# Optimization experiments

Measured on AMD Instinct MI355X. Metric: run time of the kernel, lower is better.

## Reference

```python
import jax, jax.numpy as jnp
import numpy as np

EPS = 1.1920929e-07  # torch nn.RMSNorm default eps = finfo(float32).eps
COS_EPS = 1e-8       # torch F.cosine_similarity denominator clamp

def rms_norm(x):
    # nn.RMSNorm(head_dim, elementwise_affine=False)
    return x / jnp.sqrt(jnp.mean(x * x, axis=-1, keepdims=True) + EPS)

def slerp(low, high, val):
    # spherical interpolation per last dim
    cos = jnp.sum(low * high, -1) / jnp.maximum(
        jnp.linalg.norm(low, axis=-1) * jnp.linalg.norm(high, axis=-1), COS_EPS)
    omega = jnp.arccos(jnp.clip(cos, -1.0 + 1e-7, 1.0 - 1e-7))[..., None]
    so = jnp.sin(omega)
    return (low * jnp.sin((1.0 - val) * omega) + high * jnp.sin(val * omega)) / so

def setup_inputs() -> dict:
    key = jax.random.key(0)
    k1, k2 = jax.random.split(key)
    z = jax.random.normal(k1, (8, 512, 2048), jnp.float32)          # [B, D, L]
    codebooks = rms_norm(jax.random.normal(k2, (8, 1024, 64), jnp.float32))  # [H, M, d]
    return {"z": z, "codebooks": codebooks}

def reference(z, codebooks, commitment_cost=0.25, decay=0.99):
    B, D, L = z.shape
    H, M, d = codebooks.shape
    # rearrange 'b (h d) l -> h (b l) d'
    z_split = z.reshape(B, H, d, L).transpose(1, 0, 3, 2).reshape(H, B * L, d)  # [H, N, d]

    sim = jnp.einsum('hnd,hmd->hnm', z_split, codebooks)          # [H, N, M]
    indices = jnp.argmax(sim, axis=-1)                            # [H, N]
    z_split_q = jnp.take_along_axis(codebooks, indices[:, :, None], axis=1)  # [H, N, d]

    commitment_loss = jnp.mean((jax.lax.stop_gradient(z_split) - z_split_q) ** 2)
    codebook_loss = jnp.mean((z_split - jax.lax.stop_gradient(z_split_q)) ** 2)
    vq_loss = codebook_loss + commitment_cost * commitment_loss

    # EMA slerp codebook update (training path, no_grad) -- vectorized over unique-code loop
    zs = jax.lax.stop_gradient(z_split)
    sums = jax.vmap(lambda zh, ih: jax.ops.segment_sum(zh, ih, num_segments=M))(zs, indices)  # [H, M, d]
    counts = jax.vmap(lambda ih: jax.ops.segment_sum(jnp.ones(ih.shape, zs.dtype), ih, num_segments=M))(indices)  # [H, M]
    means = sums / jnp.maximum(counts, 1.0)[..., None]
    updated = rms_norm(slerp(means, codebooks, decay))
    new_codebooks = jnp.where(counts[..., None] > 0, updated, codebooks)

    # rearrange back 'h (b l) d -> b (h d) l' and 'h (b l) -> b h l'
    z_q = z_split_q.reshape(H, B, L, d).transpose(1, 0, 3, 2).reshape(B, D, L)
    indices_out = indices.reshape(H, B, L).transpose(1, 0, 2)
    z_q = z + jax.lax.stop_gradient(z_q - z)  # straight-through
    return z_q, vq_loss, indices_out, new_codebooks
```

## Files before the change

### kernel.cpp

```cpp
#include <hip/hip_runtime.h>
#include <hip/hip_bf16.h>
#include <math.h>

#define BZ   8
#define DD   512
#define LL   2048
#define HH   8
#define MM   1024
#define DH   64
#define NN   (BZ * LL)
#define TOTAL_ELEMS (HH * NN * DH)

#define OFF_ZQ   0
#define OFF_LOSS 8388608
#define OFF_IDX  8388609
#define OFF_CB   8519681

#define CAP  128

#define WSB_SSE    0
#define WSB_CNT    64
#define WSB_LST    (64 + HH * MM * 4)
#define WSB_CBHI   (WSB_LST + HH * MM * CAP * 2)
#define WSB_CBLO   (WSB_CBHI + HH * MM * DH * 2)
#define WSB_ZS     (WSB_CBLO + HH * MM * DH * 2)
#define WS_NEED_BUCKET ((size_t)WSB_ZS + (size_t)HH * NN * DH * 4)

#define WS_PLANES_BYTE 64
#define WS_ZSPLIT_BYTE (64 + 2u * HH * MM * DH * 2)
#define WS_NEED_FAT    (WS_ZSPLIT_BYTE + (size_t)HH * NN * DH * 4)

typedef __attribute__((ext_vector_type(8))) short short8;
typedef __attribute__((ext_vector_type(4))) float float4v;

__device__ __forceinline__ unsigned short f2bf(float f) {
    unsigned int u = __builtin_bit_cast(unsigned int, f);
    u += 0x7FFFu + ((u >> 16) & 1u);
    return (unsigned short)(u >> 16);
}
__device__ __forceinline__ float bf2f(unsigned short s) {
    unsigned int u = ((unsigned int)s) << 16;
    return __builtin_bit_cast(float, u);
}

__device__ __forceinline__ void gload16(const short* g, short* l) {
    __builtin_amdgcn_global_load_lds(
        (const __attribute__((address_space(1))) unsigned int*)g,
        (__attribute__((address_space(3))) unsigned int*)l, 16, 0, 0);
}

__global__ __launch_bounds__(256) void cvt_cb_kernel(
    const float* __restrict__ cb, short* __restrict__ hip_, short* __restrict__ lop_)
{
    const int tid = blockIdx.x * 256 + threadIdx.x;
    const int c   = tid & 7;
    const int row = tid >> 3;
    const float* __restrict__ src = cb + (size_t)row * DH + c * 8;
    short hs[8], ls[8];
#pragma unroll
    for (int j = 0; j < 8; ++j) {
        const float f = src[j];
        const unsigned short hv = f2bf(f);
        hs[j] = (short)hv;
        ls[j] = (short)f2bf(f - bf2f(hv));
    }
    const int dst = row * DH + ((c ^ (row & 7)) * 8);
    *(short8*)&hip_[dst] = *(short8*)hs;
    *(short8*)&lop_[dst] = *(short8*)ls;
}

__global__ __launch_bounds__(512) void vq_assign_kernel(
    const float* __restrict__ z,
    const float* __restrict__ cb,
    const short* __restrict__ cb_hi,
    const short* __restrict__ cb_lo,
    float* __restrict__ zq_out,
    float* __restrict__ idx_out,
    float* __restrict__ sse,
    float* __restrict__ zs,
    int*   __restrict__ cnts,
    unsigned short* __restrict__ lists)
{
    __shared__ __align__(16) short hi_lds[2][64 * DH];
    __shared__ __align__(16) short lo_lds[2][64 * DH];
    __shared__ float blk_err[8];

    const int t    = threadIdx.x;
    const int h    = blockIdx.y;
    const int lane = t & 63;
    const int g    = lane >> 4;
    const int nloc = lane & 15;
    const int w    = t >> 6;

    const int r = blockIdx.x * 128 + w * 16 + nloc;
    const int b = r >> 11;
    const int l = r & (LL - 1);
    const float* __restrict__ zbase = z + ((size_t)(b * DD + h * DH) * LL + l);

    float zv[16] __attribute__((aligned(16)));
#pragma unroll
    for (int j = 0; j < 8; ++j) zv[j]     = zbase[(size_t)(g * 8 + j) * LL];
#pragma unroll
    for (int j = 0; j < 8; ++j) zv[8 + j] = zbase[(size_t)(32 + g * 8 + j) * LL];

    if (zs) {
        float* __restrict__ zr_ = zs + ((size_t)h * NN + r) * DH;
        *(float4*)&zr_[g * 8]          = *(const float4*)&zv[0];
        *(float4*)&zr_[g * 8 + 4]      = *(const float4*)&zv[4];
        *(float4*)&zr_[32 + g * 8]     = *(const float4*)&zv[8];
        *(float4*)&zr_[32 + g * 8 + 4] = *(const float4*)&zv[12];
    }

    short bh[16], bl[16];
#pragma unroll
    for (int j = 0; j < 16; ++j) {
        const unsigned short hv = f2bf(zv[j]);
        bh[j] = (short)hv;
        bl[j] = (short)f2bf(zv[j] - bf2f(hv));
    }
    const short8 Bh0 = *(short8*)&bh[0], Bh1 = *(short8*)&bh[8];
    const short8 Bl0 = *(short8*)&bl[0], Bl1 = *(short8*)&bl[8];

    const short* __restrict__ gh = cb_hi + (size_t)h * MM * DH;
    const short* __restrict__ gl = cb_lo + (size_t)h * MM * DH;

    auto stage = [&](int mt, int buf) {
        const short* sh = gh + (size_t)mt * 64 * DH;
        const short* sl = gl + (size_t)mt * 64 * DH;
        gload16(sh + t * 8, &hi_lds[buf][t * 8]);
        gload16(sl + t * 8, &lo_lds[buf][t * 8]);
    };

    stage(0, 0);

    float b1c[4], b2c[4];
    int   i1c[4], i2c[4];
#pragma unroll
    for (int s = 0; s < 4; ++s) { b1c[s] = -1e30f; b2c[s] = -1e30f; i1c[s] = 0; i2c[s] = 0; }

    const int sw8 = nloc & 7;

    for (int mt = 0; mt < MM / 64; ++mt) {
        __syncthreads();
        if (mt + 1 < MM / 64) stage(mt + 1, (mt + 1) & 1);
        const int buf = mt & 1;

#pragma unroll
        for (int s = 0; s < 4; ++s) {
            const short* hrow = &hi_lds[buf][(s * 16 + nloc) * DH];
            const short* lrow = &lo_lds[buf][(s * 16 + nloc) * DH];
            const short8 Ah0 = *(const short8*)&hrow[((g)     ^ sw8) * 8];
            const short8 Ah1 = *(const short8*)&hrow[((g + 4) ^ sw8) * 8];
            const short8 Al0 = *(const short8*)&lrow[((g)     ^ sw8) * 8];
            const short8 Al1 = *(const short8*)&lrow[((g + 4) ^ sw8) * 8];

            float4v acc = {0.f, 0.f, 0.f, 0.f};
            acc = __builtin_amdgcn_mfma_f32_16x16x32_bf16(Ah0, Bh0, acc, 0, 0, 0);
            acc = __builtin_amdgcn_mfma_f32_16x16x32_bf16(Ah1, Bh1, acc, 0, 0, 0);
            acc = __builtin_amdgcn_mfma_f32_16x16x32_bf16(Ah0, Bl0, acc, 0, 0, 0);
            acc = __builtin_amdgcn_mfma_f32_16x16x32_bf16(Ah1, Bl1, acc, 0, 0, 0);
            acc = __builtin_amdgcn_mfma_f32_16x16x32_bf16(Al0, Bh0, acc, 0, 0, 0);
            acc = __builtin_amdgcn_mfma_f32_16x16x32_bf16(Al1, Bh1, acc, 0, 0, 0);

            const int mbase = mt * 64 + s * 16 + g * 4;
#pragma unroll
            for (int reg = 0; reg < 4; ++reg) {
                const float v = acc[reg];
                const int   m = mbase + reg;
                const bool gt1 = v > b1c[s];
                const bool gt2 = v > b2c[s];
                b2c[s] = __builtin_amdgcn_fmed3f(v, b1c[s], b2c[s]);
                i2c[s] = gt1 ? i1c[s] : (gt2 ? m : i2c[s]);
                b1c[s] = fmaxf(v, b1c[s]);
                i1c[s] = gt1 ? m : i1c[s];
            }
        }
    }

    float b1 = b1c[0], b2 = b2c[0];
    int   i1 = i1c[0], i2 = i2c[0];
#pragma unroll
    for (int s = 1; s < 4; ++s) {
        const float ob1 = b1c[s], ob2 = b2c[s];
        const int   oi1 = i1c[s], oi2 = i2c[s];
        const bool agt = (b1 > ob1) || (b1 == ob1 && i1 < oi1);
        const float w1 = agt ? b1 : ob1;  const int wi1 = agt ? i1 : oi1;
        const float l1 = agt ? ob1 : b1;  const int li1 = agt ? oi1 : i1;
        const float w2 = agt ? b2 : ob2;  const int wi2 = agt ? i2 : oi2;
        const bool sgt = (l1 > w2) || (l1 == w2 && li1 < wi2);
        b1 = w1;  i1 = wi1;
        b2 = sgt ? l1 : w2;  i2 = sgt ? li1 : wi2;
    }

#pragma unroll
    for (int off = 16; off <= 32; off <<= 1) {
        float ob1 = __shfl_xor(b1, off, 64);
        int   oi1 = __shfl_xor(i1, off, 64);
        float ob2 = __shfl_xor(b2, off, 64);
        int   oi2 = __shfl_xor(i2, off, 64);
        const bool agt = (b1 > ob1) || (b1 == ob1 && i1 < oi1);
        const float w1  = agt ? b1 : ob1;  const int wi1 = agt ? i1 : oi1;
        const float l1  = agt ? ob1 : b1;  const int li1 = agt ? oi1 : i1;
        const float w2  = agt ? b2 : ob2;  const int wi2 = agt ? i2 : oi2;
        const bool sgt = (l1 > w2) || (l1 == w2 && li1 < wi2);
        b1 = w1;  i1 = wi1;
        b2 = sgt ? l1 : w2;  i2 = sgt ? li1 : wi2;
    }

    const float* __restrict__ cbh = cb + (size_t)h * MM * DH;
    const float* __restrict__ c1  = cbh + (size_t)i1 * DH;
    const float* __restrict__ c2  = cbh + (size_t)i2 * DH;
    double d1 = 0.0, d2 = 0.0;
#pragma unroll
    for (int j = 0; j < 8; ++j) {
        const int k0 = g * 8 + j, k1 = 32 + g * 8 + j;
        d1 = fma((double)zv[j],     (double)c1[k0], d1);
        d1 = fma((double)zv[8 + j], (double)c1[k1], d1);
        d2 = fma((double)zv[j],     (double)c2[k0], d2);
        d2 = fma((double)zv[8 + j], (double)c2[k1], d2);
    }
    d1 += __shfl_xor(d1, 16, 64);  d1 += __shfl_xor(d1, 32, 64);
    d2 += __shfl_xor(d2, 16, 64);  d2 += __shfl_xor(d2, 32, 64);
    const int best = (d2 > d1 || (d2 == d1 && i2 < i1)) ? i2 : i1;

    const float* __restrict__ cq  = cbh + (size_t)best * DH;
    float* __restrict__ zqp  = zq_out + ((size_t)(b * DD + h * DH) * LL + l);
    float err = 0.f;
#pragma unroll
    for (int j = 0; j < 8; ++j) {
        const int k0 = g * 8 + j, k1 = 32 + g * 8 + j;
        const float q0 = cq[k0], q1 = cq[k1];
        zqp[(size_t)k0 * LL] = q0;
        zqp[(size_t)k1 * LL] = q1;
        const float e0 = zv[j] - q0, e1 = zv[8 + j] - q1;
        err = fmaf(e0, e0, err);
        err = fmaf(e1, e1, err);
    }
    if (g == 0) {
        idx_out[((size_t)b * HH + h) * LL + l] = (float)best;
        if (cnts) {
            const int code = h * MM + best;
            const int slot = atomicAdd(&cnts[code], 1);
            if (slot < CAP) lists[(size_t)code * CAP + slot] = (unsigned short)r;
        }
    }
#pragma unroll
    for (int off = 32; off; off >>= 1) err += __shfl_xor(err, off, 64);
    if (lane == 0) blk_err[w] = err;
    __syncthreads();
    if (t == 0) {
        float s = 0.f;
#pragma unroll
        for (int i = 0; i < 8; ++i) s += blk_err[i];
        atomicAdd(sse, s);
    }
}

__global__ __launch_bounds__(256) void vq_update_kernel(
    const float* __restrict__ z,
    const float* __restrict__ zs,
    const float* __restrict__ cb,
    const float* __restrict__ idx,
    const float* __restrict__ sse,
    float* __restrict__ cb_out,
    float* __restrict__ loss_out,
    const int* __restrict__ cnts,
    const unsigned short* __restrict__ lists)
{
    if (blockIdx.x == 0 && threadIdx.x == 0) {
        loss_out[0] = 1.25f * sse[0] / (float)TOTAL_ELEMS;
    }
    const int row  = blockIdx.x * 4 + (threadIdx.x >> 6);
    const int lane = threadIdx.x & 63;
    const int h    = row >> 10;
    const int m    = row & (MM - 1);
    const float fm = (float)m;

    float acc = 0.f;
    int   cnt = 0;
    bool  fast = false;
    if (cnts) { cnt = cnts[row]; fast = (cnt <= CAP); }

    if (fast) {
        const unsigned short* __restrict__ lst = lists + (size_t)row * CAP;
        const float* __restrict__ zsh = zs + ((size_t)h * NN) * DH + lane;
        float a0 = 0.f, a1 = 0.f, a2 = 0.f, a3 = 0.f;
        int i = 0;
        for (; i + 4 <= cnt; i += 4) {
            const int n0 = lst[i], n1 = lst[i + 1], n2 = lst[i + 2], n3 = lst[i + 3];
            a0 += zsh[(size_t)n0 * DH];
            a1 += zsh[(size_t)n1 * DH];
            a2 += zsh[(size_t)n2 * DH];
            a3 += zsh[(size_t)n3 * DH];
        }
        for (; i < cnt; ++i) acc += zsh[(size_t)lst[i] * DH];
        acc += (a0 + a1) + (a2 + a3);
    } else {
        cnt = 0;
#pragma unroll 1
        for (int b = 0; b < BZ; ++b) {
            const float* __restrict__ ip  = idx + ((size_t)(b * HH + h)) * LL;
            const float* __restrict__ zb  = z + ((size_t)(b * DD + h * DH + lane)) * LL;
            const float* __restrict__ zsb = zs ? (zs + ((size_t)h * NN + (size_t)b * LL) * DH + lane)
                                              : (const float*)0;
            float4 cur = *(const float4*)(ip + lane * 4);
#pragma unroll 1
            for (int it = 0; it < LL / 256; ++it) {
                float4 nxt = cur;
                if (it + 1 < LL / 256)
                    nxt = *(const float4*)(ip + (it + 1) * 256 + lane * 4);
#pragma unroll
                for (int j = 0; j < 4; ++j) {
                    const float ivj = (&cur.x)[j];
                    unsigned long long mask = __ballot(ivj == fm);
                    cnt += (int)__popcll(mask);
                    while (mask) {
                        const int src = (int)__ffsll((long long)mask) - 1;
                        mask &= mask - 1;
                        const int l = it * 256 + src * 4 + j;
                        acc += zsb ? zsb[(size_t)l * DH]
                                   : zb[l];
                    }
                }
                cur = nxt;
            }
        }
    }

    const float cf   = (float)cnt;
    const float c    = cb[(size_t)row * DH + lane];
    const float mean = acc / fmaxf(cf, 1.0f);

    float dot = mean * c;
    float nl  = mean * mean;
    float nh  = c * c;
#pragma unroll
    for (int off = 32; off; off >>= 1) {
        dot += __shfl_xor(dot, off, 64);
        nl  += __shfl_xor(nl,  off, 64);
        nh  += __shfl_xor(nh,  off, 64);
    }

    float cosv = dot / fmaxf(sqrtf(nl) * sqrtf(nh), 1e-8f);
    cosv = fminf(fmaxf(cosv, -0.9999999f), 0.9999999f);
    const float omega = acosf(cosv);
    const float so    = sinf(omega);
    float outv = (mean * sinf(0.01f * omega) + c * sinf(0.99f * omega)) / so;

    float ms = outv * outv;
#pragma unroll
    for (int off = 32; off; off >>= 1) ms += __shfl_xor(ms, off, 64);
    ms = ms * (1.0f / (float)DH) + 1.1920929e-07f;
    const float normed = outv / sqrtf(ms);

    cb_out[(size_t)row * DH + lane] = (cnt > 0) ? normed : c;
}

extern "C" void kernel_launch(void* const* d_in, const int* in_sizes, int n_in,
                              void* d_out, int out_size, void* d_ws, size_t ws_size,
                              hipStream_t stream) {
    const float* z  = (const float*)d_in[0];
    const float* cb = (const float*)d_in[1];
    float* out = (float*)d_out;

    const bool bucket = ws_size >= WS_NEED_BUCKET;
    const bool fat    = ws_size >= WS_NEED_FAT;

    short *cb_hi, *cb_lo;
    float *zs = 0;
    int   *cnts = 0;
    unsigned short *lists = 0;

    if (bucket) {
        cnts  = (int*)((char*)d_ws + WSB_CNT);
        lists = (unsigned short*)((char*)d_ws + WSB_LST);
        cb_hi = (short*)((char*)d_ws + WSB_CBHI);
        cb_lo = (short*)((char*)d_ws + WSB_CBLO);
        zs    = (float*)((char*)d_ws + WSB_ZS);
        hipMemsetAsync(d_ws, 0, WSB_LST, stream);
    } else {
        cb_hi = (short*)((char*)d_ws + WS_PLANES_BYTE);
        cb_lo = cb_hi + (size_t)HH * MM * DH;
        zs    = fat ? (float*)((char*)d_ws + WS_ZSPLIT_BYTE) : (float*)0;
        hipMemsetAsync(d_ws, 0, 64, stream);
    }

    cvt_cb_kernel<<<(HH * MM * DH / 8) / 256, 256, 0, stream>>>(cb, cb_hi, cb_lo);

    dim3 gridA(NN / 128, HH);
    vq_assign_kernel<<<gridA, 512, 0, stream>>>(
        z, cb, cb_hi, cb_lo,
        out + OFF_ZQ, out + OFF_IDX, (float*)d_ws, zs, cnts, lists);

    dim3 gridB((HH * MM) / 4);
    vq_update_kernel<<<gridB, 256, 0, stream>>>(
        z, zs, cb, out + OFF_IDX, (float*)d_ws,
        out + OFF_CB, out + OFF_LOSS, cnts, lists);
}
```

Baseline: 190.5 us.

## Process two row tiles per wave to reuse staged codebook fragments

```diff
diff --git a/kernel.cpp b/kernel.cpp
--- a/kernel.cpp
+++ b/kernel.cpp
@@ -69,7 +69,7 @@
     *(short8*)&lop_[dst] = *(short8*)ls;
 }
 
-__global__ __launch_bounds__(512) void vq_assign_kernel(
+__global__ __launch_bounds__(512, 4) void vq_assign_kernel(
     const float* __restrict__ z,
     const float* __restrict__ cb,
     const short* __restrict__ cb_hi,
@@ -92,34 +92,39 @@
     const int nloc = lane & 15;
     const int w    = t >> 6;
 
-    const int r = blockIdx.x * 128 + w * 16 + nloc;
-    const int b = r >> 11;
-    const int l = r & (LL - 1);
-    const float* __restrict__ zbase = z + ((size_t)(b * DD + h * DH) * LL + l);
-
-    float zv[16] __attribute__((aligned(16)));
-#pragma unroll
-    for (int j = 0; j < 8; ++j) zv[j]     = zbase[(size_t)(g * 8 + j) * LL];
-#pragma unroll
-    for (int j = 0; j < 8; ++j) zv[8 + j] = zbase[(size_t)(32 + g * 8 + j) * LL];
-
-    if (zs) {
-        float* __restrict__ zr_ = zs + ((size_t)h * NN + r) * DH;
-        *(float4*)&zr_[g * 8]          = *(const float4*)&zv[0];
-        *(float4*)&zr_[g * 8 + 4]      = *(const float4*)&zv[4];
-        *(float4*)&zr_[32 + g * 8]     = *(const float4*)&zv[8];
-        *(float4*)&zr_[32 + g * 8 + 4] = *(const float4*)&zv[12];
-    }
-
-    short bh[16], bl[16];
-#pragma unroll
-    for (int j = 0; j < 16; ++j) {
-        const unsigned short hv = f2bf(zv[j]);
-        bh[j] = (short)hv;
-        bl[j] = (short)f2bf(zv[j] - bf2f(hv));
-    }
-    const short8 Bh0 = *(short8*)&bh[0], Bh1 = *(short8*)&bh[8];
-    const short8 Bl0 = *(short8*)&bl[0], Bl1 = *(short8*)&bl[8];
+    const int rbase = blockIdx.x * 256 + w * 32;
+
+    short8 Bh0[2], Bh1[2], Bl0[2], Bl1[2];
+#pragma unroll
+    for (int u = 0; u < 2; ++u) {
+        const int r = rbase + u * 16 + nloc;
+        const int b = r >> 11;
+        const int l = r & (LL - 1);
+        const float* __restrict__ zbase = z + ((size_t)(b * DD + h * DH) * LL + l);
+        float zv[16] __attribute__((aligned(16)));
+#pragma unroll
+        for (int j = 0; j < 8; ++j) zv[j]     = zbase[(size_t)(g * 8 + j) * LL];
+#pragma unroll
+        for (int j = 0; j < 8; ++j) zv[8 + j] = zbase[(size_t)(32 + g * 8 + j) * LL];
+
+        if (zs) {
+            float* __restrict__ zr_ = zs + ((size_t)h * NN + r) * DH;
+            *(float4*)&zr_[g * 8]          = *(const float4*)&zv[0];
+            *(float4*)&zr_[g * 8 + 4]      = *(const float4*)&zv[4];
+            *(float4*)&zr_[32 + g * 8]     = *(const float4*)&zv[8];
+            *(float4*)&zr_[32 + g * 8 + 4] = *(const float4*)&zv[12];
+        }
+
+        short bh[16], bl[16];
+#pragma unroll
+        for (int j = 0; j < 16; ++j) {
+            const unsigned short hv = f2bf(zv[j]);
+            bh[j] = (short)hv;
+            bl[j] = (short)f2bf(zv[j] - bf2f(hv));
+        }
+        Bh0[u] = *(short8*)&bh[0];  Bh1[u] = *(short8*)&bh[8];
+        Bl0[u] = *(short8*)&bl[0];  Bl1[u] = *(short8*)&bl[8];
+    }
 
     const short* __restrict__ gh = cb_hi + (size_t)h * MM * DH;
     const short* __restrict__ gl = cb_lo + (size_t)h * MM * DH;
@@ -136,7 +141,7 @@
     float b1c[4], b2c[4];
     int   i1c[4], i2c[4];
 #pragma unroll
-    for (int s = 0; s < 4; ++s) { b1c[s] = -1e30f; b2c[s] = -1e30f; i1c[s] = 0; i2c[s] = 0; }
+    for (int c = 0; c < 4; ++c) { b1c[c] = -1e30f; b2c[c] = -1e30f; i1c[c] = 0; i2c[c] = 0; }
 
     const int sw8 = nloc & 7;
 
@@ -154,99 +159,128 @@
             const short8 Al0 = *(const short8*)&lrow[((g)     ^ sw8) * 8];
             const short8 Al1 = *(const short8*)&lrow[((g + 4) ^ sw8) * 8];
 
-            float4v acc = {0.f, 0.f, 0.f, 0.f};
-            acc = __builtin_amdgcn_mfma_f32_16x16x32_bf16(Ah0, Bh0, acc, 0, 0, 0);
-            acc = __builtin_amdgcn_mfma_f32_16x16x32_bf16(Ah1, Bh1, acc, 0, 0, 0);
-            acc = __builtin_amdgcn_mfma_f32_16x16x32_bf16(Ah0, Bl0, acc, 0, 0, 0);
-            acc = __builtin_amdgcn_mfma_f32_16x16x32_bf16(Ah1, Bl1, acc, 0, 0, 0);
-            acc = __builtin_amdgcn_mfma_f32_16x16x32_bf16(Al0, Bh0, acc, 0, 0, 0);
-            acc = __builtin_amdgcn_mfma_f32_16x16x32_bf16(Al1, Bh1, acc, 0, 0, 0);
-
             const int mbase = mt * 64 + s * 16 + g * 4;
 #pragma unroll
-            for (int reg = 0; reg < 4; ++reg) {
-                const float v = acc[reg];
-                const int   m = mbase + reg;
-                const bool gt1 = v > b1c[s];
-                const bool gt2 = v > b2c[s];
-                b2c[s] = __builtin_amdgcn_fmed3f(v, b1c[s], b2c[s]);
-                i2c[s] = gt1 ? i1c[s] : (gt2 ? m : i2c[s]);
-                b1c[s] = fmaxf(v, b1c[s]);
-                i1c[s] = gt1 ? m : i1c[s];
+            for (int u = 0; u < 2; ++u) {
+                float4v acc = {0.f, 0.f, 0.f, 0.f};
+                acc = __builtin_amdgcn_mfma_f32_16x16x32_bf16(Ah0, Bh0[u], acc, 0, 0, 0);
+                acc = __builtin_amdgcn_mfma_f32_16x16x32_bf16(Ah1, Bh1[u], acc, 0, 0, 0);
+                acc = __builtin_amdgcn_mfma_f32_16x16x32_bf16(Ah0, Bl0[u], acc, 0, 0, 0);
+                acc = __builtin_amdgcn_mfma_f32_16x16x32_bf16(Ah1, Bl1[u], acc, 0, 0, 0);
+                acc = __builtin_amdgcn_mfma_f32_16x16x32_bf16(Al0, Bh0[u], acc, 0, 0, 0);
+                acc = __builtin_amdgcn_mfma_f32_16x16x32_bf16(Al1, Bh1[u], acc, 0, 0, 0);
+
+#pragma unroll
+                for (int reg = 0; reg < 4; ++reg) {
+                    const int   c = u * 2 + (reg & 1);
+                    const float v = acc[reg];
+                    const int   m = mbase + reg;
+                    const bool gt1 = v > b1c[c];
+                    const bool gt2 = v > b2c[c];
+                    b2c[c] = __builtin_amdgcn_fmed3f(v, b1c[c], b2c[c]);
+                    i2c[c] = gt1 ? i1c[c] : (gt2 ? m : i2c[c]);
+                    b1c[c] = fmaxf(v, b1c[c]);
+                    i1c[c] = gt1 ? m : i1c[c];
+                }
             }
         }
     }
 
-    float b1 = b1c[0], b2 = b2c[0];
-    int   i1 = i1c[0], i2 = i2c[0];
-#pragma unroll
-    for (int s = 1; s < 4; ++s) {
-        const float ob1 = b1c[s], ob2 = b2c[s];
-        const int   oi1 = i1c[s], oi2 = i2c[s];
-        const bool agt = (b1 > ob1) || (b1 == ob1 && i1 < oi1);
-        const float w1 = agt ? b1 : ob1;  const int wi1 = agt ? i1 : oi1;
-        const float l1 = agt ? ob1 : b1;  const int li1 = agt ? oi1 : i1;
-        const float w2 = agt ? b2 : ob2;  const int wi2 = agt ? i2 : oi2;
-        const bool sgt = (l1 > w2) || (l1 == w2 && li1 < wi2);
-        b1 = w1;  i1 = wi1;
-        b2 = sgt ? l1 : w2;  i2 = sgt ? li1 : wi2;
-    }
-
-#pragma unroll
-    for (int off = 16; off <= 32; off <<= 1) {
-        float ob1 = __shfl_xor(b1, off, 64);
-        int   oi1 = __shfl_xor(i1, off, 64);
-        float ob2 = __shfl_xor(b2, off, 64);
-        int   oi2 = __shfl_xor(i2, off, 64);
-        const bool agt = (b1 > ob1) || (b1 == ob1 && i1 < oi1);
-        const float w1  = agt ? b1 : ob1;  const int wi1 = agt ? i1 : oi1;
-        const float l1  = agt ? ob1 : b1;  const int li1 = agt ? oi1 : i1;
-        const float w2  = agt ? b2 : ob2;  const int wi2 = agt ? i2 : oi2;
-        const bool sgt = (l1 > w2) || (l1 == w2 && li1 < wi2);
-        b1 = w1;  i1 = wi1;
-        b2 = sgt ? l1 : w2;  i2 = sgt ? li1 : wi2;
-    }
-
     const float* __restrict__ cbh = cb + (size_t)h * MM * DH;
-    const float* __restrict__ c1  = cbh + (size_t)i1 * DH;
-    const float* __restrict__ c2  = cbh + (size_t)i2 * DH;
-    double d1 = 0.0, d2 = 0.0;
-#pragma unroll
-    for (int j = 0; j < 8; ++j) {
-        const int k0 = g * 8 + j, k1 = 32 + g * 8 + j;
-        d1 = fma((double)zv[j],     (double)c1[k0], d1);
-        d1 = fma((double)zv[8 + j], (double)c1[k1], d1);
-        d2 = fma((double)zv[j],     (double)c2[k0], d2);
-        d2 = fma((double)zv[8 + j], (double)c2[k1], d2);
-    }
-    d1 += __shfl_xor(d1, 16, 64);  d1 += __shfl_xor(d1, 32, 64);
-    d2 += __shfl_xor(d2, 16, 64);  d2 += __shfl_xor(d2, 32, 64);
-    const int best = (d2 > d1 || (d2 == d1 && i2 < i1)) ? i2 : i1;
-
-    const float* __restrict__ cq  = cbh + (size_t)best * DH;
-    float* __restrict__ zqp  = zq_out + ((size_t)(b * DD + h * DH) * LL + l);
-    float err = 0.f;
-#pragma unroll
-    for (int j = 0; j < 8; ++j) {
-        const int k0 = g * 8 + j, k1 = 32 + g * 8 + j;
-        const float q0 = cq[k0], q1 = cq[k1];
-        zqp[(size_t)k0 * LL] = q0;
-        zqp[(size_t)k1 * LL] = q1;
-        const float e0 = zv[j] - q0, e1 = zv[8 + j] - q1;
-        err = fmaf(e0, e0, err);
-        err = fmaf(e1, e1, err);
-    }
-    if (g == 0) {
-        idx_out[((size_t)b * HH + h) * LL + l] = (float)best;
-        if (cnts) {
-            const int code = h * MM + best;
-            const int slot = atomicAdd(&cnts[code], 1);
-            if (slot < CAP) lists[(size_t)code * CAP + slot] = (unsigned short)r;
-        }
-    }
-#pragma unroll
-    for (int off = 32; off; off >>= 1) err += __shfl_xor(err, off, 64);
-    if (lane == 0) blk_err[w] = err;
+    float err_total = 0.f;
+
+#pragma unroll
+    for (int u = 0; u < 2; ++u) {
+        float b1 = b1c[u * 2], b2 = b2c[u * 2];
+        int   i1 = i1c[u * 2], i2 = i2c[u * 2];
+        {
+            const float ob1 = b1c[u * 2 + 1], ob2 = b2c[u * 2 + 1];
+            const int   oi1 = i1c[u * 2 + 1], oi2 = i2c[u * 2 + 1];
+            const bool agt = (b1 > ob1) || (b1 == ob1 && i1 < oi1);
+            const float w1 = agt ? b1 : ob1;  const int wi1 = agt ? i1 : oi1;
+            const float l1 = agt ? ob1 : b1;  const int li1 = agt ? oi1 : i1;
+            const float w2 = agt ? b2 : ob2;  const int wi2 = agt ? i2 : oi2;
+            const bool sgt = (l1 > w2) || (l1 == w2 && li1 < wi2);
+            b1 = w1;  i1 = wi1;
+            b2 = sgt ? l1 : w2;  i2 = sgt ? li1 : wi2;
+        }
+
+#pragma unroll
+        for (int off = 16; off <= 32; off <<= 1) {
+            float ob1 = __shfl_xor(b1, off, 64);
+            int   oi1 = __shfl_xor(i1, off, 64);
+            float ob2 = __shfl_xor(b2, off, 64);
+            int   oi2 = __shfl_xor(i2, off, 64);
+            const bool agt = (b1 > ob1) || (b1 == ob1 && i1 < oi1);
+            const float w1  = agt ? b1 : ob1;  const int wi1 = agt ? i1 : oi1;
+            const float l1  = agt ? ob1 : b1;  const int li1 = agt ? oi1 : i1;
+            const float w2  = agt ? b2 : ob2;  const int wi2 = agt ? i2 : oi2;
+            const bool sgt = (l1 > w2) || (l1 == w2 && li1 < wi2);
+            b1 = w1;  i1 = wi1;
+            b2 = sgt ? l1 : w2;  i2 = sgt ? li1 : wi2;
+        }
+
+        const int r = rbase + u * 16 + nloc;
+        const int b = r >> 11;
+        const int l = r & (LL - 1);
+
+        float zr[16] __attribute__((aligned(16)));
+        if (zs) {
+            const float* __restrict__ zp = zs + ((size_t)h * NN + r) * DH;
+            *(float4*)&zr[0]  = *(const float4*)&zp[g * 8];
+            *(float4*)&zr[4]  = *(const float4*)&zp[g * 8 + 4];
+            *(float4*)&zr[8]  = *(const float4*)&zp[32 + g * 8];
+            *(float4*)&zr[12] = *(const float4*)&zp[32 + g * 8 + 4];
+        } else {
+            const float* __restrict__ zbase = z + ((size_t)(b * DD + h * DH) * LL + l);
+#pragma unroll
+            for (int j = 0; j < 8; ++j) zr[j]     = zbase[(size_t)(g * 8 + j) * LL];
+#pragma unroll
+            for (int j = 0; j < 8; ++j) zr[8 + j] = zbase[(size_t)(32 + g * 8 + j) * LL];
+        }
+
+        const float* __restrict__ c1 = cbh + (size_t)i1 * DH;
+        const float* __restrict__ c2 = cbh + (size_t)i2 * DH;
+        double d1 = 0.0, d2 = 0.0;
+#pragma unroll
+        for (int j = 0; j < 8; ++j) {
+            const int k0 = g * 8 + j, k1 = 32 + g * 8 + j;
+            d1 = fma((double)zr[j],     (double)c1[k0], d1);
+            d1 = fma((double)zr[8 + j], (double)c1[k1], d1);
+            d2 = fma((double)zr[j],     (double)c2[k0], d2);
+            d2 = fma((double)zr[8 + j], (double)c2[k1], d2);
+        }
+        d1 += __shfl_xor(d1, 16, 64);  d1 += __shfl_xor(d1, 32, 64);
+        d2 += __shfl_xor(d2, 16, 64);  d2 += __shfl_xor(d2, 32, 64);
+        const int best = (d2 > d1 || (d2 == d1 && i2 < i1)) ? i2 : i1;
+
+        const float* __restrict__ cq = cbh + (size_t)best * DH;
+        float* __restrict__ zqp = zq_out + ((size_t)(b * DD + h * DH) * LL + l);
+        float err = 0.f;
+#pragma unroll
+        for (int j = 0; j < 8; ++j) {
+            const int k0 = g * 8 + j, k1 = 32 + g * 8 + j;
+            const float q0 = cq[k0], q1 = cq[k1];
+            zqp[(size_t)k0 * LL] = q0;
+            zqp[(size_t)k1 * LL] = q1;
+            const float e0 = zr[j] - q0, e1 = zr[8 + j] - q1;
+            err = fmaf(e0, e0, err);
+            err = fmaf(e1, e1, err);
+        }
+        if (g == 0) {
+            idx_out[((size_t)b * HH + h) * LL + l] = (float)best;
+            if (cnts) {
+                const int code = h * MM + best;
+                const int slot = atomicAdd(&cnts[code], 1);
+                if (slot < CAP) lists[(size_t)code * CAP + slot] = (unsigned short)r;
+            }
+        }
+        err_total += err;
+    }
+
+#pragma unroll
+    for (int off = 32; off; off >>= 1) err_total += __shfl_xor(err_total, off, 64);
+    if (lane == 0) blk_err[w] = err_total;
     __syncthreads();
     if (t == 0) {
         float s = 0.f;
@@ -387,7 +421,7 @@
 
     cvt_cb_kernel<<<(HH * MM * DH / 8) / 256, 256, 0, stream>>>(cb, cb_hi, cb_lo);
 
-    dim3 gridA(NN / 128, HH);
+    dim3 gridA(NN / 256, HH);
     vq_assign_kernel<<<gridA, 512, 0, stream>>>(
         z, cb, cb_hi, cb_lo,
         out + OFF_ZQ, out + OFF_IDX, (float*)d_ws, zs, cnts, lists);
```

Measured after the change: 195.3 us. +2.5%, slower.
